# Kernel tuning notes

Measured on AMD Instinct MI355X. Metric: run time of the kernel, lower is better.

Reference implementation:

```python
import jax, jax.numpy as jnp
import numpy as np

D_SCALE = 1000.0  # quantization scale for the int32 motion-magnitude depth key


def _forward_warp_max_motion(im0, flow, eps):
    """Depth-tested forward splatting (Sanchez et al. 2013, Alg. 3, max-motion variant).

    Each source pixel is bilinearly splatted to the 4 integer neighbors of its
    flow-displaced target. A scatter-max on quantized motion magnitude acts as the
    depth test; only contributions whose motion equals the per-pixel max are
    accumulated (deterministic two-pass version of the atomic CUDA kernel).
    """
    B, C, H, W = im0.shape
    fx, fy = flow[..., 0], flow[..., 1]
    x = jnp.arange(W, dtype=flow.dtype)[None, None, :] + fx  # [B,H,W] target x
    y = jnp.arange(H, dtype=flow.dtype)[None, :, None] + fy  # [B,H,W] target y
    x0 = jnp.floor(x)
    y0 = jnp.floor(y)
    ax = x - x0  # fractional parts -> bilinear weights
    ay = y - y0
    x0i = x0.astype(jnp.int32)
    y0i = y0.astype(jnp.int32)
    corners = [
        (x0i,     y0i,     (1.0 - ax) * (1.0 - ay)),
        (x0i + 1, y0i,     ax * (1.0 - ay)),
        (x0i,     y0i + 1, (1.0 - ax) * ay),
        (x0i + 1, y0i + 1, ax * ay),
    ]
    d = jnp.round(jnp.sqrt(fx * fx + fy * fy) * D_SCALE).astype(jnp.int32)  # [B,H,W]
    boff = (jnp.arange(B, dtype=jnp.int32) * (H * W))[:, None, None]
    idxs, ws, ds = [], [], []
    for tx, ty, w in corners:
        valid = (tx >= 0) & (tx < W) & (ty >= 0) & (ty < H)
        idx = jnp.where(valid, boff + ty * W + tx, 0)
        idxs.append(idx.reshape(-1))
        ws.append(jnp.where(valid, w, 0.0).reshape(-1))
        ds.append(jnp.where(valid, d, -1).reshape(-1))
    idx = jnp.concatenate(idxs)        # [4*B*H*W]
    wv = jnp.concatenate(ws)
    dv = jnp.concatenate(ds)
    N = B * H * W
    # pass 1: scatter-max depth buffer (init 0, as in the torch code)
    dbuf = jnp.zeros(N, jnp.int32).at[idx].max(dv)
    # pass 2: accumulate only depth-test winners
    win = (dv >= 0) & (dv == dbuf[idx])
    w_eff = jnp.where(win, wv, 0.0)
    wght = jnp.zeros(N, im0.dtype).at[idx].add(w_eff)  # kernel adds w per channel then /C == w once
    src = im0.transpose(1, 0, 2, 3).reshape(C, N)      # [C, N]
    vals = jnp.tile(src, (1, 4)) * w_eff[None, :]      # [C, 4N], corner-major matches idx
    im1buf = jnp.zeros((C, N), im0.dtype).at[:, idx].add(vals)
    wght_b = wght.reshape(B, 1, H, W)
    im1buf_b = im1buf.reshape(C, B, H, W).transpose(1, 0, 2, 3)
    im1 = im1buf_b / jnp.clip(wght_b, eps, None)
    disocclusions = (wght_b == 0).astype(im0.dtype)
    return im1, disocclusions, dbuf.reshape(B, 1, H, W)


def setup_inputs() -> dict:
    key = jax.random.key(0)
    k1, k2 = jax.random.split(key)
    B, C, H, W = 4, 3, 1080, 1920
    im0 = jax.random.uniform(k1, (B, C, H, W), dtype=jnp.float32)
    flow = jax.random.normal(k2, (B, H, W, 2), dtype=jnp.float32) * 20.0  # ~20 px motions
    return {"im0": im0, "flow": flow}


def reference(im0, flow):
    eps = 1e-05
    im1, _, _ = _forward_warp_max_motion(im0, flow, eps)
    return im1
```

## Files before the change

### kernel.cpp

```cpp
#include <hip/hip_runtime.h>

static constexpr int B = 4, C = 3, H = 1080, W = 1920;
static constexpr int HW = H * W;
static constexpr int NPIX = B * HW;
static constexpr int BLOCK = 256;

static constexpr int TW = 64, TH = 32;
static constexpr int TPX = TW * TH;
static constexpr int TXN = W / TW;
static constexpr int TYN = (H + TH - 1) / TH;
static constexpr int NT = TXN * TYN;
static constexpr int CAP = 4096;
static constexpr int OFL_CAP = 65536;
static constexpr int BPB = HW / BLOCK;

__device__ __forceinline__ int depth_key(float fx, float fy) {
    float m2 = __fadd_rn(__fmul_rn(fx, fx), __fmul_rn(fy, fy));
    return (int)rintf(__fmul_rn(sqrtf(m2), 1000.0f));
}

__global__ __launch_bounds__(BLOCK) void k_bin(const float2* __restrict__ flow,
                                               int* __restrict__ cnt,
                                               int* __restrict__ bin,
                                               int* __restrict__ ofl_cnt,
                                               int* __restrict__ ofl_i,
                                               int* __restrict__ ofl_t,
                                               int* __restrict__ dbuf) {
    __shared__ int hcnt[NT];
    __shared__ int hbase[NT];
    const int tid = threadIdx.x;
    for (int j = tid; j < NT; j += BLOCK) hcnt[j] = 0;
    __syncthreads();

    const int b = blockIdx.x / BPB;
    const int i = blockIdx.x * BLOCK + tid;
    const int pix = i - b * HW;
    const int h = pix / W;
    const int w = pix - h * W;
    const float2 f = flow[i];
    const float x = (float)w + f.x;
    const float y = (float)h + f.y;
    const int x0 = (int)floorf(x);
    const int y0 = (int)floorf(y);

    int tl[4], rk[4]; int ntl = 0;
    #pragma unroll
    for (int dy = 0; dy < 2; ++dy) {
        int cy = y0 + dy;
        if ((unsigned)cy >= (unsigned)H) continue;
        #pragma unroll
        for (int dx = 0; dx < 2; ++dx) {
            int cx = x0 + dx;
            if ((unsigned)cx >= (unsigned)W) continue;
            int t = (cy >> 5) * TXN + (cx >> 6);
            bool dup = false;
            for (int k = 0; k < ntl; ++k) dup |= (tl[k] == t);
            if (dup) continue;
            tl[ntl] = t;
            rk[ntl] = atomicAdd(&hcnt[t], 1);
            ++ntl;
        }
    }
    __syncthreads();

    for (int j = tid; j < NT; j += BLOCK) {
        int c = hcnt[j];
        if (c > 0) hbase[j] = atomicAdd(&cnt[b * NT + j], c);
    }
    __syncthreads();

    bool did_depth_fb = false;
    for (int k = 0; k < ntl; ++k) {
        int t = tl[k];
        int slot = hbase[t] + rk[k];
        if (slot < CAP) {
            bin[(size_t)(b * NT + t) * CAP + slot] = pix;
        } else {
            int pos = atomicAdd(ofl_cnt, 1);
            if (pos < OFL_CAP) { ofl_i[pos] = i; ofl_t[pos] = t; }
            if (!did_depth_fb) {
                did_depth_fb = true;
                int d = depth_key(f.x, f.y);
                #pragma unroll
                for (int yy = 0; yy < 2; ++yy) {
                    int cy2 = y0 + yy;
                    if ((unsigned)cy2 >= (unsigned)H) continue;
                    #pragma unroll
                    for (int xx = 0; xx < 2; ++xx) {
                        int cx2 = x0 + xx;
                        if ((unsigned)cx2 >= (unsigned)W) continue;
                        atomicMax(&dbuf[b * HW + cy2 * W + cx2], d);
                    }
                }
            }
        }
    }
}

__global__ __launch_bounds__(BLOCK) void k_tile(const float* __restrict__ im0,
                                                const float2* __restrict__ flow,
                                                const int* __restrict__ cnt,
                                                const int* __restrict__ bin,
                                                const int* __restrict__ ofl_cnt,
                                                int* __restrict__ dbuf,
                                                float* __restrict__ wght,
                                                float* __restrict__ out) {
    __shared__ int   dmax[TPX];
    __shared__ float acc[4][TPX];
    const int tid = threadIdx.x;
    const int bx = blockIdx.x, by = blockIdx.y, b = blockIdx.z;
    const int tx0 = bx * TW, ty0 = by * TH;
    const int t = by * TXN + bx;
    int* db = dbuf + (size_t)b * HW;

    for (int i = tid; i < TPX; i += BLOCK) {
        int gy = ty0 + (i >> 6), gx = tx0 + (i & 63);
        dmax[i] = (gy < H) ? db[gy * W + gx] : 0;
        acc[0][i] = 0.0f; acc[1][i] = 0.0f; acc[2][i] = 0.0f; acc[3][i] = 0.0f;
    }
    __syncthreads();

    const int n = min(cnt[b * NT + t], CAP);
    const int* mybin = bin + (size_t)(b * NT + t) * CAP;
    const float2* fb = flow + (size_t)b * HW;

    for (int e = tid; e < n; e += BLOCK) {
        int pix = mybin[e];
        int h = pix / W, w = pix - h * W;
        float2 f = fb[pix];
        float x = (float)w + f.x;
        float y = (float)h + f.y;
        int x0 = (int)floorf(x);
        int y0 = (int)floorf(y);
        int d = depth_key(f.x, f.y);
        #pragma unroll
        for (int dy = 0; dy < 2; ++dy) {
            int cy = y0 + dy;
            if ((cy >> 5) != by || cy >= H) continue;
            #pragma unroll
            for (int dx = 0; dx < 2; ++dx) {
                int cx = x0 + dx;
                if ((cx >> 6) != bx) continue;
                atomicMax(&dmax[((cy - ty0) << 6) + (cx - tx0)], d);
            }
        }
    }
    __syncthreads();

    for (int i = tid; i < TPX; i += BLOCK) {
        int gy = ty0 + (i >> 6), gx = tx0 + (i & 63);
        if (gy < H) db[gy * W + gx] = dmax[i];
    }

    const float* ib = im0 + (size_t)b * C * HW;
    for (int e = tid; e < n; e += BLOCK) {
        int pix = mybin[e];
        int h = pix / W, w = pix - h * W;
        float2 f = fb[pix];
        float x = (float)w + f.x;
        float y = (float)h + f.y;
        float x0f = floorf(x), y0f = floorf(y);
        int x0 = (int)x0f, y0 = (int)y0f;
        float ax = __fsub_rn(x, x0f);
        float ay = __fsub_rn(y, y0f);
        int d = depth_key(f.x, f.y);
        float wxv[2] = { __fsub_rn(1.0f, ax), ax };
        float wyv[2] = { __fsub_rn(1.0f, ay), ay };
        int   locs[4]; float lw[4]; int nw = 0;
        #pragma unroll
        for (int dy = 0; dy < 2; ++dy) {
            int cy = y0 + dy;
            if ((cy >> 5) != by || cy >= H) continue;
            #pragma unroll
            for (int dx = 0; dx < 2; ++dx) {
                int cx = x0 + dx;
                if ((cx >> 6) != bx) continue;
                int loc = ((cy - ty0) << 6) + (cx - tx0);
                if (dmax[loc] != d) continue;
                locs[nw] = loc;
                lw[nw] = __fmul_rn(wxv[dx], wyv[dy]);
                ++nw;
            }
        }
        if (nw) {
            float c0 = ib[pix];
            float c1 = ib[pix + HW];
            float c2 = ib[pix + 2 * HW];
            for (int k = 0; k < nw; ++k) {
                int p = locs[k]; float wg = lw[k];
                atomicAdd(&acc[0][p], wg);
                atomicAdd(&acc[1][p], __fmul_rn(c0, wg));
                atomicAdd(&acc[2][p], __fmul_rn(c1, wg));
                atomicAdd(&acc[3][p], __fmul_rn(c2, wg));
            }
        }
    }
    __syncthreads();

    const bool raw = (*ofl_cnt) > 0;
    float* ob = out + (size_t)b * C * HW;
    float* wb = wght + (size_t)b * HW;
    for (int i = tid; i < TPX; i += BLOCK) {
        int gy = ty0 + (i >> 6), gx = tx0 + (i & 63);
        if (gy >= H) continue;
        int g = gy * W + gx;
        float a0 = acc[0][i], a1 = acc[1][i], a2 = acc[2][i], a3 = acc[3][i];
        if (raw) {
            wb[g] = a0;
            ob[g] = a1; ob[g + HW] = a2; ob[g + 2 * HW] = a3;
        } else {
            float wv = fmaxf(a0, 1e-5f);
            ob[g]          = __fdiv_rn(a1, wv);
            ob[g + HW]     = __fdiv_rn(a2, wv);
            ob[g + 2 * HW] = __fdiv_rn(a3, wv);
        }
    }
}

__global__ __launch_bounds__(BLOCK) void k_accum_ofl(const float* __restrict__ im0,
                                                     const float2* __restrict__ flow,
                                                     const int* __restrict__ ofl_cnt,
                                                     const int* __restrict__ ofl_i,
                                                     const int* __restrict__ ofl_t,
                                                     const int* __restrict__ dbuf,
                                                     float* __restrict__ wght,
                                                     float* __restrict__ out) {
    int k = blockIdx.x * BLOCK + threadIdx.x;
    int n = min(*ofl_cnt, OFL_CAP);
    if (k >= n) return;
    int i = ofl_i[k], t = ofl_t[k];
    int b = i / HW;
    int pix = i - b * HW;
    int h = pix / W, w = pix - h * W;
    int bx = t % TXN, by = t / TXN;
    float2 f = flow[i];
    float x = (float)w + f.x;
    float y = (float)h + f.y;
    float x0f = floorf(x), y0f = floorf(y);
    int x0 = (int)x0f, y0 = (int)y0f;
    float ax = __fsub_rn(x, x0f);
    float ay = __fsub_rn(y, y0f);
    int d = depth_key(f.x, f.y);
    const float* src = im0 + (size_t)b * C * HW + pix;
    float c0 = src[0], c1 = src[HW], c2 = src[2 * HW];
    float wxv[2] = { __fsub_rn(1.0f, ax), ax };
    float wyv[2] = { __fsub_rn(1.0f, ay), ay };
    #pragma unroll
    for (int dy = 0; dy < 2; ++dy) {
        int cy = y0 + dy;
        if ((cy >> 5) != by || cy >= H) continue;
        #pragma unroll
        for (int dx = 0; dx < 2; ++dx) {
            int cx = x0 + dx;
            if ((cx >> 6) != bx) continue;
            int idx = b * HW + cy * W + cx;
            if (dbuf[idx] != d) continue;
            float wg = __fmul_rn(wxv[dx], wyv[dy]);
            atomicAdd(&wght[idx], wg);
            float* o = out + (size_t)b * C * HW + cy * W + cx;
            atomicAdd(&o[0],      __fmul_rn(c0, wg));
            atomicAdd(&o[HW],     __fmul_rn(c1, wg));
            atomicAdd(&o[2 * HW], __fmul_rn(c2, wg));
        }
    }
}

__global__ __launch_bounds__(BLOCK) void k_norm(float* __restrict__ out,
                                                const float* __restrict__ wght,
                                                const int* __restrict__ ofl_cnt) {
    if (*ofl_cnt == 0) return;
    int i = blockIdx.x * BLOCK + threadIdx.x;
    if (i >= NPIX) return;
    int b = i / HW;
    int pix = i - b * HW;
    float wv = fmaxf(wght[i], 1e-5f);
    float* o = out + (size_t)b * C * HW + pix;
    o[0]      = __fdiv_rn(o[0], wv);
    o[HW]     = __fdiv_rn(o[HW], wv);
    o[2 * HW] = __fdiv_rn(o[2 * HW], wv);
}

extern "C" void kernel_launch(void* const* d_in, const int* in_sizes, int n_in,
                              void* d_out, int out_size, void* d_ws, size_t ws_size,
                              hipStream_t stream) {
    const float*  im0  = (const float*)d_in[0];
    const float2* flow = (const float2*)d_in[1];
    float* out = (float*)d_out;

    char* ws = (char*)d_ws;
    int*   dbuf    = (int*)ws;
    float* wght    = (float*)(ws + (size_t)NPIX * 4);
    int*   cnt     = (int*)(ws + (size_t)NPIX * 8);
    int*   ofl_cnt = cnt + B * NT;
    int*   ofl_i   = ofl_cnt + 1;
    int*   ofl_t   = ofl_i + OFL_CAP;
    int*   bin     = ofl_t + OFL_CAP;

    hipMemsetAsync(dbuf, 0, (size_t)NPIX * 4, stream);
    hipMemsetAsync(cnt, 0, (size_t)(B * NT + 1) * 4, stream);

    int lgrid = NPIX / BLOCK;
    dim3 tgrid(TXN, TYN, B);

    k_bin      <<<lgrid, BLOCK, 0, stream>>>(flow, cnt, bin, ofl_cnt, ofl_i, ofl_t, dbuf);
    k_tile     <<<tgrid, BLOCK, 0, stream>>>(im0, flow, cnt, bin, ofl_cnt, dbuf, wght, out);
    k_accum_ofl<<<OFL_CAP / BLOCK, BLOCK, 0, stream>>>(im0, flow, ofl_cnt, ofl_i, ofl_t, dbuf, wght, out);
    k_norm     <<<lgrid, BLOCK, 0, stream>>>(out, wght, ofl_cnt);
}
```

Baseline: 523.7 us.

## Store precomputed splat entries in bins and shrink tiles to 32x32

Bins now hold a float4 per entry with target x, y, pixel index and depth key, so the tile kernel no longer re-reads flow or recomputes the coordinates and depth. Tiles shrink from 64x32 to 32x32 with a smaller per-tile capacity, which cuts LDS use enough to request higher occupancy. The tile kernel skips reading and writing the global depth buffer when nothing overflowed, and the LDS accumulator becomes interleaved float4. The trade-offs are four times more bin storage traffic per entry, more duplicated boundary entries with smaller tiles, and a higher chance of hitting the overflow path.

```diff
diff --git a/kernel.cpp b/kernel.cpp
--- a/kernel.cpp
+++ b/kernel.cpp
@@ -5,12 +5,12 @@
 static constexpr int NPIX = B * HW;
 static constexpr int BLOCK = 256;
 
-static constexpr int TW = 64, TH = 32;
+static constexpr int TW = 32, TH = 32;
 static constexpr int TPX = TW * TH;
 static constexpr int TXN = W / TW;
 static constexpr int TYN = (H + TH - 1) / TH;
 static constexpr int NT = TXN * TYN;
-static constexpr int CAP = 4096;
+static constexpr int CAP = 1536;
 static constexpr int OFL_CAP = 65536;
 static constexpr int BPB = HW / BLOCK;
 
@@ -21,7 +21,7 @@
 
 __global__ __launch_bounds__(BLOCK) void k_bin(const float2* __restrict__ flow,
                                                int* __restrict__ cnt,
-                                               int* __restrict__ bin,
+                                               float4* __restrict__ bin,
                                                int* __restrict__ ofl_cnt,
                                                int* __restrict__ ofl_i,
                                                int* __restrict__ ofl_t,
@@ -29,19 +29,22 @@
     __shared__ int hcnt[NT];
     __shared__ int hbase[NT];
     const int tid = threadIdx.x;
-    for (int j = tid; j < NT; j += BLOCK) hcnt[j] = 0;
-    __syncthreads();
 
     const int b = blockIdx.x / BPB;
     const int i = blockIdx.x * BLOCK + tid;
+    const float2 f = flow[i];
+
+    for (int j = tid; j < NT; j += BLOCK) hcnt[j] = 0;
+    __syncthreads();
+
     const int pix = i - b * HW;
     const int h = pix / W;
     const int w = pix - h * W;
-    const float2 f = flow[i];
     const float x = (float)w + f.x;
     const float y = (float)h + f.y;
     const int x0 = (int)floorf(x);
     const int y0 = (int)floorf(y);
+    const int d = depth_key(f.x, f.y);
 
     int tl[4], rk[4]; int ntl = 0;
     #pragma unroll
@@ -52,7 +55,7 @@
         for (int dx = 0; dx < 2; ++dx) {
             int cx = x0 + dx;
             if ((unsigned)cx >= (unsigned)W) continue;
-            int t = (cy >> 5) * TXN + (cx >> 6);
+            int t = (cy >> 5) * TXN + (cx >> 5);
             bool dup = false;
             for (int k = 0; k < ntl; ++k) dup |= (tl[k] == t);
             if (dup) continue;
@@ -69,18 +72,18 @@
     }
     __syncthreads();
 
+    const float4 entry = make_float4(x, y, __int_as_float(pix), __int_as_float(d));
     bool did_depth_fb = false;
     for (int k = 0; k < ntl; ++k) {
         int t = tl[k];
         int slot = hbase[t] + rk[k];
         if (slot < CAP) {
-            bin[(size_t)(b * NT + t) * CAP + slot] = pix;
+            bin[(size_t)(b * NT + t) * CAP + slot] = entry;
         } else {
             int pos = atomicAdd(ofl_cnt, 1);
             if (pos < OFL_CAP) { ofl_i[pos] = i; ofl_t[pos] = t; }
             if (!did_depth_fb) {
                 did_depth_fb = true;
-                int d = depth_key(f.x, f.y);
                 #pragma unroll
                 for (int yy = 0; yy < 2; ++yy) {
                     int cy2 = y0 + yy;
@@ -97,42 +100,38 @@
     }
 }
 
-__global__ __launch_bounds__(BLOCK) void k_tile(const float* __restrict__ im0,
-                                                const float2* __restrict__ flow,
-                                                const int* __restrict__ cnt,
-                                                const int* __restrict__ bin,
-                                                const int* __restrict__ ofl_cnt,
-                                                int* __restrict__ dbuf,
-                                                float* __restrict__ wght,
-                                                float* __restrict__ out) {
-    __shared__ int   dmax[TPX];
-    __shared__ float acc[4][TPX];
+__global__ __launch_bounds__(BLOCK, 8) void k_tile(const float* __restrict__ im0,
+                                                   const int* __restrict__ cnt,
+                                                   const float4* __restrict__ bin,
+                                                   const int* __restrict__ ofl_cnt,
+                                                   int* __restrict__ dbuf,
+                                                   float* __restrict__ wght,
+                                                   float* __restrict__ out) {
+    __shared__ int    dmax[TPX];
+    __shared__ float4 accv[TPX];
+    float* accf = (float*)accv;
     const int tid = threadIdx.x;
     const int bx = blockIdx.x, by = blockIdx.y, b = blockIdx.z;
     const int tx0 = bx * TW, ty0 = by * TH;
     const int t = by * TXN + bx;
+    const bool have_ofl = (*ofl_cnt) > 0;
     int* db = dbuf + (size_t)b * HW;
 
     for (int i = tid; i < TPX; i += BLOCK) {
-        int gy = ty0 + (i >> 6), gx = tx0 + (i & 63);
-        dmax[i] = (gy < H) ? db[gy * W + gx] : 0;
-        acc[0][i] = 0.0f; acc[1][i] = 0.0f; acc[2][i] = 0.0f; acc[3][i] = 0.0f;
+        int gy = ty0 + (i >> 5), gx = tx0 + (i & 31);
+        dmax[i] = (have_ofl && gy < H) ? db[gy * W + gx] : 0;
+        accv[i] = make_float4(0.0f, 0.0f, 0.0f, 0.0f);
     }
     __syncthreads();
 
     const int n = min(cnt[b * NT + t], CAP);
-    const int* mybin = bin + (size_t)(b * NT + t) * CAP;
-    const float2* fb = flow + (size_t)b * HW;
+    const float4* mybin = bin + (size_t)(b * NT + t) * CAP;
 
     for (int e = tid; e < n; e += BLOCK) {
-        int pix = mybin[e];
-        int h = pix / W, w = pix - h * W;
-        float2 f = fb[pix];
-        float x = (float)w + f.x;
-        float y = (float)h + f.y;
-        int x0 = (int)floorf(x);
-        int y0 = (int)floorf(y);
-        int d = depth_key(f.x, f.y);
+        float4 en = mybin[e];
+        int x0 = (int)floorf(en.x);
+        int y0 = (int)floorf(en.y);
+        int d = __float_as_int(en.w);
         #pragma unroll
         for (int dy = 0; dy < 2; ++dy) {
             int cy = y0 + dy;
@@ -140,30 +139,29 @@
             #pragma unroll
             for (int dx = 0; dx < 2; ++dx) {
                 int cx = x0 + dx;
-                if ((cx >> 6) != bx) continue;
-                atomicMax(&dmax[((cy - ty0) << 6) + (cx - tx0)], d);
+                if ((cx >> 5) != bx) continue;
+                atomicMax(&dmax[((cy - ty0) << 5) + (cx - tx0)], d);
             }
         }
     }
     __syncthreads();
 
-    for (int i = tid; i < TPX; i += BLOCK) {
-        int gy = ty0 + (i >> 6), gx = tx0 + (i & 63);
-        if (gy < H) db[gy * W + gx] = dmax[i];
+    if (have_ofl) {
+        for (int i = tid; i < TPX; i += BLOCK) {
+            int gy = ty0 + (i >> 5), gx = tx0 + (i & 31);
+            if (gy < H) db[gy * W + gx] = dmax[i];
+        }
     }
 
     const float* ib = im0 + (size_t)b * C * HW;
     for (int e = tid; e < n; e += BLOCK) {
-        int pix = mybin[e];
-        int h = pix / W, w = pix - h * W;
-        float2 f = fb[pix];
-        float x = (float)w + f.x;
-        float y = (float)h + f.y;
-        float x0f = floorf(x), y0f = floorf(y);
+        float4 en = mybin[e];
+        float x0f = floorf(en.x), y0f = floorf(en.y);
         int x0 = (int)x0f, y0 = (int)y0f;
-        float ax = __fsub_rn(x, x0f);
-        float ay = __fsub_rn(y, y0f);
-        int d = depth_key(f.x, f.y);
+        float ax = __fsub_rn(en.x, x0f);
+        float ay = __fsub_rn(en.y, y0f);
+        int pix = __float_as_int(en.z);
+        int d   = __float_as_int(en.w);
         float wxv[2] = { __fsub_rn(1.0f, ax), ax };
         float wyv[2] = { __fsub_rn(1.0f, ay), ay };
         int   locs[4]; float lw[4]; int nw = 0;
@@ -174,8 +172,8 @@
             #pragma unroll
             for (int dx = 0; dx < 2; ++dx) {
                 int cx = x0 + dx;
-                if ((cx >> 6) != bx) continue;
-                int loc = ((cy - ty0) << 6) + (cx - tx0);
+                if ((cx >> 5) != bx) continue;
+                int loc = ((cy - ty0) << 5) + (cx - tx0);
                 if (dmax[loc] != d) continue;
                 locs[nw] = loc;
                 lw[nw] = __fmul_rn(wxv[dx], wyv[dy]);
@@ -188,31 +186,30 @@
             float c2 = ib[pix + 2 * HW];
             for (int k = 0; k < nw; ++k) {
                 int p = locs[k]; float wg = lw[k];
-                atomicAdd(&acc[0][p], wg);
-                atomicAdd(&acc[1][p], __fmul_rn(c0, wg));
-                atomicAdd(&acc[2][p], __fmul_rn(c1, wg));
-                atomicAdd(&acc[3][p], __fmul_rn(c2, wg));
+                atomicAdd(&accf[4 * p + 0], wg);
+                atomicAdd(&accf[4 * p + 1], __fmul_rn(c0, wg));
+                atomicAdd(&accf[4 * p + 2], __fmul_rn(c1, wg));
+                atomicAdd(&accf[4 * p + 3], __fmul_rn(c2, wg));
             }
         }
     }
     __syncthreads();
 
-    const bool raw = (*ofl_cnt) > 0;
     float* ob = out + (size_t)b * C * HW;
     float* wb = wght + (size_t)b * HW;
     for (int i = tid; i < TPX; i += BLOCK) {
-        int gy = ty0 + (i >> 6), gx = tx0 + (i & 63);
+        int gy = ty0 + (i >> 5), gx = tx0 + (i & 31);
         if (gy >= H) continue;
         int g = gy * W + gx;
-        float a0 = acc[0][i], a1 = acc[1][i], a2 = acc[2][i], a3 = acc[3][i];
-        if (raw) {
-            wb[g] = a0;
-            ob[g] = a1; ob[g + HW] = a2; ob[g + 2 * HW] = a3;
+        float4 a = accv[i];
+        if (have_ofl) {
+            wb[g] = a.x;
+            ob[g] = a.y; ob[g + HW] = a.z; ob[g + 2 * HW] = a.w;
         } else {
-            float wv = fmaxf(a0, 1e-5f);
-            ob[g]          = __fdiv_rn(a1, wv);
-            ob[g + HW]     = __fdiv_rn(a2, wv);
-            ob[g + 2 * HW] = __fdiv_rn(a3, wv);
+            float wv = fmaxf(a.x, 1e-5f);
+            ob[g]          = __fdiv_rn(a.y, wv);
+            ob[g + HW]     = __fdiv_rn(a.z, wv);
+            ob[g + 2 * HW] = __fdiv_rn(a.w, wv);
         }
     }
 }
@@ -252,7 +249,7 @@
         #pragma unroll
         for (int dx = 0; dx < 2; ++dx) {
             int cx = x0 + dx;
-            if ((cx >> 6) != bx) continue;
+            if ((cx >> 5) != bx) continue;
             int idx = b * HW + cy * W + cx;
             if (dbuf[idx] != d) continue;
             float wg = __fmul_rn(wxv[dx], wyv[dy]);
@@ -269,15 +266,16 @@
                                                 const float* __restrict__ wght,
                                                 const int* __restrict__ ofl_cnt) {
     if (*ofl_cnt == 0) return;
-    int i = blockIdx.x * BLOCK + threadIdx.x;
-    if (i >= NPIX) return;
-    int b = i / HW;
-    int pix = i - b * HW;
-    float wv = fmaxf(wght[i], 1e-5f);
-    float* o = out + (size_t)b * C * HW + pix;
-    o[0]      = __fdiv_rn(o[0], wv);
-    o[HW]     = __fdiv_rn(o[HW], wv);
-    o[2 * HW] = __fdiv_rn(o[2 * HW], wv);
+    for (int i = blockIdx.x * BLOCK + threadIdx.x; i < NPIX;
+         i += gridDim.x * BLOCK) {
+        int b = i / HW;
+        int pix = i - b * HW;
+        float wv = fmaxf(wght[i], 1e-5f);
+        float* o = out + (size_t)b * C * HW + pix;
+        o[0]      = __fdiv_rn(o[0], wv);
+        o[HW]     = __fdiv_rn(o[HW], wv);
+        o[2 * HW] = __fdiv_rn(o[2 * HW], wv);
+    }
 }
 
 extern "C" void kernel_launch(void* const* d_in, const int* in_sizes, int n_in,
@@ -288,13 +286,14 @@
     float* out = (float*)d_out;
 
     char* ws = (char*)d_ws;
-    int*   dbuf    = (int*)ws;
-    float* wght    = (float*)(ws + (size_t)NPIX * 4);
-    int*   cnt     = (int*)(ws + (size_t)NPIX * 8);
+    float4* bin = (float4*)ws;
+    const size_t bin_bytes = (size_t)B * NT * CAP * sizeof(float4);
+    int*   dbuf    = (int*)(ws + bin_bytes);
+    float* wght    = (float*)(ws + bin_bytes + (size_t)NPIX * 4);
+    int*   cnt     = (int*)(ws + bin_bytes + (size_t)NPIX * 8);
     int*   ofl_cnt = cnt + B * NT;
     int*   ofl_i   = ofl_cnt + 1;
     int*   ofl_t   = ofl_i + OFL_CAP;
-    int*   bin     = ofl_t + OFL_CAP;
 
     hipMemsetAsync(dbuf, 0, (size_t)NPIX * 4, stream);
     hipMemsetAsync(cnt, 0, (size_t)(B * NT + 1) * 4, stream);
@@ -303,7 +302,7 @@
     dim3 tgrid(TXN, TYN, B);
 
     k_bin      <<<lgrid, BLOCK, 0, stream>>>(flow, cnt, bin, ofl_cnt, ofl_i, ofl_t, dbuf);
-    k_tile     <<<tgrid, BLOCK, 0, stream>>>(im0, flow, cnt, bin, ofl_cnt, dbuf, wght, out);
+    k_tile     <<<tgrid, BLOCK, 0, stream>>>(im0, cnt, bin, ofl_cnt, dbuf, wght, out);
     k_accum_ofl<<<OFL_CAP / BLOCK, BLOCK, 0, stream>>>(im0, flow, ofl_cnt, ofl_i, ofl_t, dbuf, wght, out);
-    k_norm     <<<lgrid, BLOCK, 0, stream>>>(out, wght, ofl_cnt);
-}
+    k_norm     <<<2048, BLOCK, 0, stream>>>(out, wght, ofl_cnt);
+}
```

Result: faster. 453.0 us (-13.5%).
